# Performance work log

Measured on AMD Instinct MI355X. Metric: run time of the kernel, lower is better.

## Reference

```python
import jax, jax.numpy as jnp
import numpy as np

N_QUBITS = 8


def _rot_mats(p):
    # p: (n, 3) -> per-qubit 2x2 unitary RX(p2) @ RZ(p1) @ RY(p0), shape (n, 2, 2)
    a, b, c = 0.5 * p[:, 0], 0.5 * p[:, 1], 0.5 * p[:, 2]
    zc = jnp.zeros_like(a).astype(jnp.complex64)
    ca, sa = jnp.cos(a), jnp.sin(a)
    ry = jnp.stack([jnp.stack([ca, -sa], -1), jnp.stack([sa, ca], -1)], -2).astype(jnp.complex64)
    eb = jnp.exp(-1j * b)
    rz = jnp.stack([jnp.stack([eb, zc], -1), jnp.stack([zc, jnp.conj(eb)], -1)], -2)
    cc = jnp.cos(c).astype(jnp.complex64)
    sc = -1j * jnp.sin(c)
    rx = jnp.stack([jnp.stack([cc, sc], -1), jnp.stack([sc, cc], -1)], -2)
    return rx @ rz @ ry


def _qgate(x, params):
    # Batched statevector simulation of the PennyLane circuit.
    # x: (B, n) RX-encoding angles; params: (depth, n, 3). Wire 0 = most-significant bit.
    B, n = x.shape
    half = 0.5 * x
    # RX(x)|0> per qubit = [cos(x/2), -i sin(x/2)]
    amps = jnp.stack([jnp.cos(half).astype(jnp.complex64), (-1j) * jnp.sin(half)], axis=-1)  # (B,n,2)
    state = amps[:, 0]  # (B, 2)
    for q in range(1, n):
        state = (state[:, :, None] * amps[:, q][:, None, :]).reshape(B, -1)
    for d in range(params.shape[0]):
        U = _rot_mats(params[d])  # (n, 2, 2)
        for w in range(n):
            s = state.reshape(B, 2 ** w, 2, -1)
            s = jnp.einsum('ab,xlbr->xlar', U[w], s)
            state = s.reshape(B, -1)
        for c in range(n - 1):  # CNOT chain (c controls c+1)
            s = state.reshape(B, 2 ** c, 2, 2, -1)
            s = jnp.stack([s[:, :, 0], s[:, :, 1, ::-1]], axis=2)
            state = s.reshape(B, -1)
    probs = state.real ** 2 + state.imag ** 2  # (B, 2**n)
    k = np.arange(2 ** n)
    signs = (1.0 - 2.0 * (((k[None, :] >> (n - 1 - np.arange(n)[:, None])) & 1))).astype(np.float32)
    return probs @ jnp.asarray(signs).T  # (B, n) Pauli-Z expvals


def _apply_gate_list(x, params_list):
    # params_list: (n_gates, depth, n, 3); gates applied sequentially
    for g in range(params_list.shape[0]):
        x = _qgate(x, params_list[g])
    return x


def setup_inputs() -> dict:
    key = jax.random.key(0)
    ks = jax.random.split(key, 10)
    T, B, D, H, P, NQ, DP = 32, 64, 512, 512, 64, N_QUBITS, 2
    inputs = jax.random.normal(ks[0], (T, B, D), jnp.float32)
    W_proj = jax.random.normal(ks[1], (P, D + H), jnp.float32) / jnp.sqrt(jnp.float32(D + H))
    b_proj = jax.random.normal(ks[2], (P,), jnp.float32) * 0.01
    W_toq = jax.random.normal(ks[3], (NQ, P), jnp.float32) / jnp.sqrt(jnp.float32(P))
    W_q2h = jax.random.normal(ks[4], (H, NQ), jnp.float32) / jnp.sqrt(jnp.float32(NQ))
    f_params = jax.random.normal(ks[5], (DP, DP, NQ, 3), jnp.float32)
    i_params = jax.random.normal(ks[6], (DP, DP, NQ, 3), jnp.float32)
    g_params = jax.random.normal(ks[7], (DP, DP, NQ, 3), jnp.float32)
    o_params = jax.random.normal(ks[8], (DP, DP, NQ, 3), jnp.float32)
    return dict(inputs=inputs, W_proj=W_proj, b_proj=b_proj, W_toq=W_toq, W_q2h=W_q2h,
                f_params=f_params, i_params=i_params, g_params=g_params, o_params=o_params)


def reference(inputs, W_proj, b_proj, W_toq, W_q2h, f_params, i_params, g_params, o_params):
    B = inputs.shape[1]
    H = W_q2h.shape[0]

    def step(carry, x):
        hx, cx = carry
        combined = jnp.concatenate([x, hx], axis=1)          # (B, D+H)
        proj = combined @ W_proj.T + b_proj                   # (B, P)
        qin = proj @ W_toq.T                                  # (B, NQ)
        f = jax.nn.sigmoid(_apply_gate_list(qin, f_params) @ W_q2h.T)
        i = jax.nn.sigmoid(_apply_gate_list(qin, i_params) @ W_q2h.T)
        g = jnp.tanh(_apply_gate_list(qin, g_params) @ W_q2h.T)
        o = jax.nn.sigmoid(_apply_gate_list(qin, o_params) @ W_q2h.T)
        cx2 = f * cx + i * g
        hx2 = o * jnp.tanh(cx2)
        return (hx2, cx2), hx2

    init = (jnp.zeros((B, H), inputs.dtype), jnp.zeros((B, H), inputs.dtype))
    (hx, cx), stacked = jax.lax.scan(step, init, inputs)
    return stacked, hx, cx
```

## Files before the change

kernel.cpp:

```cpp
#include <hip/hip_runtime.h>
#include <math.h>

#define T_STEPS 32
#define BATCH 64

#define WS_WXQ 0
#define WS_WHQ 4096
#define WS_BQ  8192
#define WS_U   8208
#define WS_XQ  9232
#define WS_AB  25616

typedef float v2f __attribute__((ext_vector_type(2)));
typedef unsigned int u32x2 __attribute__((ext_vector_type(2)));
typedef __fp16 half4v __attribute__((ext_vector_type(4)));
typedef float f32x4 __attribute__((ext_vector_type(4)));

struct c32 { float x, y; };
__device__ __forceinline__ c32 cmul(c32 a, c32 b){ return {a.x*b.x - a.y*b.y, a.x*b.y + a.y*b.x}; }
__device__ __forceinline__ c32 cadd(c32 a, c32 b){ return {a.x+b.x, a.y+b.y}; }

__device__ __forceinline__ v2f mkv(float x, float y){ v2f r; r.x = x; r.y = y; return r; }
__device__ __forceinline__ v2f cmulv(v2f a, v2f b){
    return mkv(a.x, a.x) * b + mkv(-a.y, a.y) * mkv(b.y, b.x);
}
__device__ __forceinline__ float fast_sigmoid(float x){ return 1.f/(1.f + __expf(-x)); }
__device__ __forceinline__ float fast_tanh(float x){ float e = __expf(2.f*x); return 1.f - 2.f/(e+1.f); }

template<int C> __device__ __forceinline__ float dppf(float v){
    return __int_as_float(__builtin_amdgcn_mov_dpp(__float_as_int(v), C, 0xF, 0xF, true));
}
__device__ __forceinline__ float swap16(float v, int lane){
#if __has_builtin(__builtin_amdgcn_permlane16_swap)
    u32x2 r = __builtin_amdgcn_permlane16_swap(__float_as_uint(v), __float_as_uint(v), false, false);
    return __uint_as_float((lane & 16) ? r.x : r.y);
#else
    return __shfl_xor(v, 16);
#endif
}
__device__ __forceinline__ float swap32(float v, int lane){
#if __has_builtin(__builtin_amdgcn_permlane32_swap)
    u32x2 r = __builtin_amdgcn_permlane32_swap(__float_as_uint(v), __float_as_uint(v), false, false);
    return __uint_as_float((lane & 32) ? r.x : r.y);
#else
    return __shfl_xor(v, 32);
#endif
}
template<int LM> __device__ __forceinline__ float lanexor(float v, int lane){
    if constexpr (LM == 1)       return dppf<0xB1>(v);
    else if constexpr (LM == 2)  return dppf<0x4E>(v);
    else if constexpr (LM == 4)  return dppf<0x1B>(dppf<0x141>(v));
    else if constexpr (LM == 8)  return dppf<0x128>(v);
    else if constexpr (LM == 16) return swap16(v, lane);
    else                         return swap32(v, lane);
}
__device__ __forceinline__ float rdl(float v, int l){
    return __int_as_float(__builtin_amdgcn_readlane(__float_as_int(v), l));
}
__device__ __forceinline__ void fsincos(float rev, float* s, float* c){
#if __has_builtin(__builtin_amdgcn_sinf) && __has_builtin(__builtin_amdgcn_cosf)
    *s = __builtin_amdgcn_sinf(rev);
    *c = __builtin_amdgcn_cosf(rev);
#else
    __sincosf(rev * 6.2831853071795864f, s, c);
#endif
}

__device__ __forceinline__ void rot_u(const float* p3, float* dst){
    float a = 0.5f * p3[0], b = 0.5f * p3[1], c = 0.5f * p3[2];
    float ca = cosf(a), sa = sinf(a);
    float cb = cosf(b), sb = sinf(b);
    float cc = cosf(c), sc = sinf(c);
    c32 eb  = {cb, -sb};
    c32 ebc = {cb,  sb};
    c32 scx = {0.f, -sc};
    c32 m00 = { eb.x * ca,  eb.y * ca};
    c32 m01 = {-eb.x * sa, -eb.y * sa};
    c32 m10 = { ebc.x * sa, ebc.y * sa};
    c32 m11 = { ebc.x * ca, ebc.y * ca};
    c32 U00 = cadd(c32{cc * m00.x, cc * m00.y}, cmul(scx, m10));
    c32 U01 = cadd(c32{cc * m01.x, cc * m01.y}, cmul(scx, m11));
    c32 U10 = cadd(cmul(scx, m00), c32{cc * m10.x, cc * m10.y});
    c32 U11 = cadd(cmul(scx, m01), c32{cc * m11.x, cc * m11.y});
    dst[0] = U00.x; dst[1] = U00.y; dst[2] = U01.x; dst[3] = U01.y;
    dst[4] = U10.x; dst[5] = U10.y; dst[6] = U11.x; dst[7] = U11.y;
}

__global__ void precompute_kernel(const float* __restrict__ W_proj,
                                  const float* __restrict__ b_proj,
                                  const float* __restrict__ W_toq,
                                  const float* __restrict__ fP, const float* __restrict__ iP,
                                  const float* __restrict__ gP, const float* __restrict__ oP,
                                  float* __restrict__ ws)
{
    int tid = threadIdx.x;
    int blk = blockIdx.x;
    if (blk < 32) {
        int idx = blk * 256 + tid;
        int q = idx >> 10, dd = idx & 1023;
        float acc = 0.f;
        for (int p = 0; p < 64; ++p) acc += W_toq[q * 64 + p] * W_proj[p * 1024 + dd];
        if (dd < 512) ws[WS_WXQ + q * 512 + dd] = acc;
        else          ws[WS_WHQ + q * 512 + (dd - 512)] = acc;
        if (idx < 8) {
            float a2 = 0.f;
            for (int p = 0; p < 64; ++p) a2 += W_toq[idx * 64 + p] * b_proj[p];
            ws[WS_BQ + idx] = a2;
        }
    } else if (blk == 32) {
        if (tid < 128) {
            int gt = tid >> 5, rest = tid & 31;
            const float* P = (gt == 0) ? fP : (gt == 1) ? iP : (gt == 2) ? gP : oP;
            int g = (rest >> 4) & 1, d = (rest >> 3) & 1, w = rest & 7;
            rot_u(P + (((g * 2 + d) * 8 + w) * 3), ws + WS_U + tid * 8);
        }
    } else {
        __shared__ float sW[8][8];
        int combo = blk - 33;
        int gt = combo >> 1, gl = combo & 1;
        if (tid < 8) {
            const float* P = (gt == 0) ? fP : (gt == 1) ? iP : (gt == 2) ? gP : oP;
            rot_u(P + (((gl * 2 + 1) * 8 + tid) * 3), &sW[tid][0]);
        }
        __syncthreads();
        int rp = tid >> 4, rr = tid & 15;
        c32 pa = {1.f, 0.f};
        #pragma unroll
        for (int w = 0; w < 4; ++w) {
            int i = (rp >> (3 - w)) & 1, j = (rr >> (3 - w)) & 1;
            c32 e = {sW[w][(i * 2 + j) * 2], sW[w][(i * 2 + j) * 2 + 1]};
            pa = cmul(pa, e);
        }
        ws[WS_AB + combo * 1024 + tid * 2]     = pa.x;
        ws[WS_AB + combo * 1024 + tid * 2 + 1] = pa.y;
        c32 pb = {1.f, 0.f};
        #pragma unroll
        for (int w = 4; w < 8; ++w) {
            int i = (rp >> (7 - w)) & 1, j = (rr >> (7 - w)) & 1;
            c32 e = {sW[w][(i * 2 + j) * 2], sW[w][(i * 2 + j) * 2 + 1]};
            pb = cmul(pb, e);
        }
        ws[WS_AB + combo * 1024 + 512 + tid * 2]     = pb.x;
        ws[WS_AB + combo * 1024 + 512 + tid * 2 + 1] = pb.y;
    }
}

__global__ void xq_kernel(const float* __restrict__ inputs, float* __restrict__ ws)
{
    __shared__ float xs[512];
    int row = blockIdx.x;
    int tid = threadIdx.x;
    xs[tid]       = inputs[row * 512 + tid];
    xs[tid + 256] = inputs[row * 512 + 256 + tid];
    __syncthreads();
    int g = tid >> 5, j = tid & 31;
    const float* w = ws + WS_WXQ + g * 512;
    float acc = 0.f;
    #pragma unroll 4
    for (int i = 0; i < 16; ++i) acc += xs[j + 32 * i] * w[j + 32 * i];
    acc += __shfl_xor(acc, 1);  acc += __shfl_xor(acc, 2);
    acc += __shfl_xor(acc, 4);  acc += __shfl_xor(acc, 8);
    acc += __shfl_xor(acc, 16);
    if (j == 0) ws[WS_XQ + row * 8 + g] = acc + ws[WS_BQ + g];
}

__global__ __launch_bounds__(256, 1)
void recurrence_kernel(const float* __restrict__ W_q2h,
                       const float* __restrict__ ws,
                       float* __restrict__ out)
{
    __shared__ __align__(16) float sU[1024];
    __shared__ __align__(16) float sXq[T_STEPS * 8];
    __shared__ __align__(16) float sexpW[4][8];
    __shared__ __align__(16) float qpartW[4][8];
    __shared__ __align__(16) float sH[T_STEPS * 512];

    int tid = threadIdx.x;
    int b   = blockIdx.x;
    int wv  = tid >> 6;
    int lane = tid & 63;
    int l = lane;

    for (int i = tid; i < 1024; i += 256) sU[i] = ws[WS_U + i];
    sXq[tid] = ws[WS_XQ + ((tid >> 3) * 64 + b) * 8 + (tid & 7)];
    if (tid < 32) ((float*)qpartW)[tid] = 0.f;

    v2f wha2[4], whb2[4];
    #pragma unroll
    for (int j = 0; j < 4; ++j) {
        wha2[j] = mkv(ws[WS_WHQ + (2*j) * 512 + tid],       ws[WS_WHQ + (2*j+1) * 512 + tid]);
        whb2[j] = mkv(ws[WS_WHQ + (2*j) * 512 + tid + 256], ws[WS_WHQ + (2*j+1) * 512 + tid + 256]);
    }
    v2f w2hp[8];
    {
        float4 a0 = *(const float4*)&W_q2h[tid * 8];
        float4 a1 = *(const float4*)&W_q2h[tid * 8 + 4];
        float4 b0 = *(const float4*)&W_q2h[(tid + 256) * 8];
        float4 b1 = *(const float4*)&W_q2h[(tid + 256) * 8 + 4];
        w2hp[0] = mkv(a0.x, b0.x); w2hp[1] = mkv(a0.y, b0.y);
        w2hp[2] = mkv(a0.z, b0.z); w2hp[3] = mkv(a0.w, b0.w);
        w2hp[4] = mkv(a1.x, b1.x); w2hp[5] = mkv(a1.y, b1.y);
        w2hp[6] = mkv(a1.z, b1.z); w2hp[7] = mkv(a1.w, b1.w);
    }

    half4v ArT[2], AiT[2], nAiT[2], Brf[2], Bif[2], nBif[2];
    {
        int q4 = lane >> 4, n = lane & 15;
        #pragma unroll
        for (int gl = 0; gl < 2; ++gl) {
            const float* Ab = ws + WS_AB + (wv * 2 + gl) * 1024;
            const float* Bb = Ab + 512;
            #pragma unroll
            for (int j = 0; j < 4; ++j) {
                int k = 4 * q4 + j;
                float ar = Ab[(n * 16 + k) * 2], ai = Ab[(n * 16 + k) * 2 + 1];
                float br = Bb[(n * 16 + k) * 2], bi = Bb[(n * 16 + k) * 2 + 1];
                ArT[gl][j]  = (__fp16)ar;  AiT[gl][j] = (__fp16)ai;  nAiT[gl][j] = (__fp16)(-ai);
                Brf[gl][j]  = (__fp16)br;  Bif[gl][j] = (__fp16)bi;  nBif[gl][j] = (__fp16)(-bi);
            }
        }
    }

    __syncthreads();

    v2f sA0[2], sB0[2], sA1[2], sB1[2], sA5[2], sB5[2], sA6[2], sB6[2], sA7[2], sB7[2];
    v2f A2a[2], B2a[2], A2b[2], B2b[2];
    v2f A3a[2], B3a[2], A3b[2], B3b[2];
    v2f A4a[2], B4a[2], A4b[2], B4b[2];
    {
        int s0 = (l >> 5) & 1;
        int s1 = ((l >> 5) ^ (l >> 4)) & 1;
        int s5 = ((l >> 3) ^ (l >> 2)) & 1;
        int s6 = ((l >> 2) ^ (l >> 1)) & 1;
        int s7 = ((l >> 1) ^ l) & 1;
        int L4 = (l >> 4) & 1;
        int L3 = (l >> 3) & 1;
        #pragma unroll
        for (int gl = 0; gl < 2; ++gl) {
            const float* d0 = sU + (wv * 32 + gl * 16) * 8;
            auto colA = [&](int q, int c){ const float* m = d0 + q * 8 + c * 4; return mkv(m[0], m[1]); };
            auto colB = [&](int q, int c){ const float* m = d0 + q * 8 + c * 4; return mkv(m[3 - c * 4 + c * 4 + 3 - 3 + 3], 0.f); };
            #define CA(q,c) mkv(d0[(q)*8 + (c)*4 + 0], d0[(q)*8 + (c)*4 + 1])
            #define CB(q,c) mkv(d0[(q)*8 + (c)*4 + 3], -d0[(q)*8 + (c)*4 + 2])
            sA0[gl] = s0 ? CA(0,1) : CA(0,0);  sB0[gl] = s0 ? CB(0,1) : CB(0,0);
            sA1[gl] = s1 ? CA(1,1) : CA(1,0);  sB1[gl] = s1 ? CB(1,1) : CB(1,0);
            sA5[gl] = s5 ? CA(5,1) : CA(5,0);  sB5[gl] = s5 ? CB(5,1) : CB(5,0);
            sA6[gl] = s6 ? CA(6,1) : CA(6,0);  sB6[gl] = s6 ? CB(6,1) : CB(6,0);
            sA7[gl] = s7 ? CA(7,1) : CA(7,0);  sB7[gl] = s7 ? CB(7,1) : CB(7,0);
            A2a[gl] = L4 ? CA(2,1) : CA(2,0);  B2a[gl] = L4 ? CB(2,1) : CB(2,0);
            A2b[gl] = L4 ? CA(2,0) : CA(2,1);  B2b[gl] = L4 ? CB(2,0) : CB(2,1);
            A3a[gl] = CA(3,0);                 B3a[gl] = CB(3,0);
            A3b[gl] = CA(3,1);                 B3b[gl] = CB(3,1);
            A4a[gl] = L3 ? CA(4,1) : CA(4,0);  B4a[gl] = L3 ? CB(4,1) : CB(4,0);
            A4b[gl] = L3 ? CA(4,0) : CA(4,1);  B4b[gl] = L3 ? CB(4,0) : CB(4,1);
            #undef CA
            #undef CB
            (void)colA; (void)colB;
        }
    }
    float sg[6];
    #pragma unroll
    for (int st = 0; st < 6; ++st) sg[st] = ((l >> st) & 1) ? -1.f : 1.f;

    const float REVC = 0.07957747154594767f;
    const f32x4 zacc = {0.f, 0.f, 0.f, 0.f};
    float c0 = 0.f, c1 = 0.f, h0 = 0.f, h1 = 0.f;

    for (int t = 0; t < T_STEPS; ++t) {
        float ang[8];
        {
            const v2f* qw = (const v2f*)qpartW;
            const v2f* xq2 = (const v2f*)&sXq[t * 8];
            #pragma unroll
            for (int j = 0; j < 4; ++j) {
                v2f s_ = ((qw[j] + qw[4 + j]) + (qw[8 + j] + qw[12 + j]) + xq2[j]) * REVC;
                ang[2 * j] = s_.x; ang[2 * j + 1] = s_.y;
            }
        }

        float e[8];
        #pragma unroll
        for (int gl = 0; gl < 2; ++gl) {
            float sh[8], ch[8];
            #pragma unroll
            for (int q = 0; q < 8; ++q) fsincos(ang[q], &sh[q], &ch[q]);

            v2f u0 = ch[0] * sA0[gl] + sh[0] * sB0[gl];
            v2f u1 = ch[1] * sA1[gl] + sh[1] * sB1[gl];
            v2f u5 = ch[5] * sA5[gl] + sh[5] * sB5[gl];
            v2f u6 = ch[6] * sA6[gl] + sh[6] * sB6[gl];
            v2f u7 = ch[7] * sA7[gl] + sh[7] * sB7[gl];
            v2f u2a = ch[2] * A2a[gl] + sh[2] * B2a[gl];
            v2f u2b = ch[2] * A2b[gl] + sh[2] * B2b[gl];
            v2f u3a = ch[3] * A3a[gl] + sh[3] * B3a[gl];
            v2f u3b = ch[3] * A3b[gl] + sh[3] * B3b[gl];
            v2f u4a = ch[4] * A4a[gl] + sh[4] * B4a[gl];
            v2f u4b = ch[4] * A4b[gl] + sh[4] * B4b[gl];

            v2f hi = cmulv(u0, u1);
            v2f lo = cmulv(cmulv(u5, u6), u7);
            v2f hilo = cmulv(hi, lo);
            v2f u23_0 = cmulv(u2a, u3a);
            v2f u23_1 = cmulv(u2a, u3b);
            v2f u23_2 = cmulv(u2b, u3b);
            v2f u23_3 = cmulv(u2b, u3a);
            v2f mid0 = cmulv(u23_0, u4a);
            v2f mid1 = cmulv(u23_1, u4b);
            v2f mid2 = cmulv(u23_2, u4a);
            v2f mid3 = cmulv(u23_3, u4b);
            v2f a0 = cmulv(hilo, mid0);
            v2f a1 = cmulv(hilo, mid1);
            v2f a2 = cmulv(hilo, mid2);
            v2f a3 = cmulv(hilo, mid3);

            half4v Sr, Si;
            Sr[0] = (__fp16)a0.x; Sr[1] = (__fp16)a1.x; Sr[2] = (__fp16)a2.x; Sr[3] = (__fp16)a3.x;
            Si[0] = (__fp16)a0.y; Si[1] = (__fp16)a1.y; Si[2] = (__fp16)a2.y; Si[3] = (__fp16)a3.y;

            f32x4 TrT = __builtin_amdgcn_mfma_f32_16x16x16f16(Sr, ArT[gl], zacc, 0, 0, 0);
            TrT = __builtin_amdgcn_mfma_f32_16x16x16f16(Si, nAiT[gl], TrT, 0, 0, 0);
            f32x4 TiT = __builtin_amdgcn_mfma_f32_16x16x16f16(Sr, AiT[gl], zacc, 0, 0, 0);
            TiT = __builtin_amdgcn_mfma_f32_16x16x16f16(Si, ArT[gl], TiT, 0, 0, 0);
            half4v TrH, TiH;
            #pragma unroll
            for (int j = 0; j < 4; ++j) { TrH[j] = (__fp16)TrT[j]; TiH[j] = (__fp16)TiT[j]; }
            f32x4 Xr = __builtin_amdgcn_mfma_f32_16x16x16f16(Brf[gl], TrH, zacc, 0, 0, 0);
            Xr = __builtin_amdgcn_mfma_f32_16x16x16f16(nBif[gl], TiH, Xr, 0, 0, 0);
            f32x4 Xi = __builtin_amdgcn_mfma_f32_16x16x16f16(Brf[gl], TiH, zacc, 0, 0, 0);
            Xi = __builtin_amdgcn_mfma_f32_16x16x16f16(Bif[gl], TrH, Xi, 0, 0, 0);

            float p0 = Xr[0]*Xr[0] + Xi[0]*Xi[0];
            float p1 = Xr[1]*Xr[1] + Xi[1]*Xi[1];
            float p2 = Xr[2]*Xr[2] + Xi[2]*Xi[2];
            float p3 = Xr[3]*Xr[3] + Xi[3]*Xi[3];
            float w0v = (p0 + p1) + (p2 + p3);
            float w6v = (p0 + p1) - (p2 + p3);
            float w7v = (p0 - p1) - (p2 - p3);
            #define WHT_STAGE(LM, ST) { float v_; \
                v_ = lanexor<LM>(w0v, lane); w0v = __builtin_fmaf(sg[ST], w0v, v_); \
                v_ = lanexor<LM>(w6v, lane); w6v = __builtin_fmaf(sg[ST], w6v, v_); \
                v_ = lanexor<LM>(w7v, lane); w7v = __builtin_fmaf(sg[ST], w7v, v_); }
            WHT_STAGE(1, 0) WHT_STAGE(2, 1) WHT_STAGE(4, 2)
            WHT_STAGE(8, 3) WHT_STAGE(16, 4) WHT_STAGE(32, 5)
            #undef WHT_STAGE
            e[0] = rdl(w0v, 8);  e[1] = rdl(w0v, 12); e[2] = rdl(w0v, 14);
            e[3] = rdl(w0v, 15); e[4] = rdl(w0v, 47); e[5] = rdl(w0v, 63);
            e[6] = rdl(w6v, 63); e[7] = rdl(w7v, 63);
            if (gl == 0) {
                #pragma unroll
                for (int q = 0; q < 8; ++q) ang[q] = e[q] * REVC;
            }
        }
        if (lane == 0) {
            float4 e0v; e0v.x = e[0]; e0v.y = e[1]; e0v.z = e[2]; e0v.w = e[3];
            float4 e1v; e1v.x = e[4]; e1v.y = e[5]; e1v.z = e[6]; e1v.w = e[7];
            *(float4*)&sexpW[wv][0] = e0v;
            *(float4*)&sexpW[wv][4] = e1v;
        }
        __syncthreads();

        {
            v2f pre[4];
            #pragma unroll
            for (int g = 0; g < 4; ++g) {
                float4 ea = *(const float4*)&sexpW[g][0];
                float4 eb2 = *(const float4*)&sexpW[g][4];
                v2f acc = ea.x * w2hp[0] + ea.y * w2hp[1] + ea.z * w2hp[2] + ea.w * w2hp[3]
                        + eb2.x * w2hp[4] + eb2.y * w2hp[5] + eb2.z * w2hp[6] + eb2.w * w2hp[7];
                pre[g] = acc;
            }
            float f0 = fast_sigmoid(pre[0].x), i0 = fast_sigmoid(pre[1].x);
            float g0 = fast_tanh(pre[2].x),    o0 = fast_sigmoid(pre[3].x);
            c0 = f0 * c0 + i0 * g0;  h0 = o0 * fast_tanh(c0);
            float f1 = fast_sigmoid(pre[0].y), i1 = fast_sigmoid(pre[1].y);
            float g1 = fast_tanh(pre[2].y),    o1 = fast_sigmoid(pre[3].y);
            c1 = f1 * c1 + i1 * g1;  h1 = o1 * fast_tanh(c1);
            sH[t * 512 + tid]       = h0;
            sH[t * 512 + tid + 256] = h1;
        }

        {
            v2f pp[4];
            #pragma unroll
            for (int j = 0; j < 4; ++j) pp[j] = wha2[j] * h0 + whb2[j] * h1;
            #pragma unroll
            for (int j = 0; j < 4; ++j) {
                pp[j] += mkv(lanexor<1>(pp[j].x, lane), lanexor<1>(pp[j].y, lane));
                pp[j] += mkv(lanexor<2>(pp[j].x, lane), lanexor<2>(pp[j].y, lane));
                pp[j] += mkv(lanexor<4>(pp[j].x, lane), lanexor<4>(pp[j].y, lane));
            }
            int sel = lane & 7;
            float y = (sel == 0) ? pp[0].x : (sel == 1) ? pp[0].y
                    : (sel == 2) ? pp[1].x : (sel == 3) ? pp[1].y
                    : (sel == 4) ? pp[2].x : (sel == 5) ? pp[2].y
                    : (sel == 6) ? pp[3].x : pp[3].y;
            y += lanexor<8>(y, lane);
            y += swap16(y, lane);
            y += swap32(y, lane);
            if (lane < 8) qpartW[wv][lane] = y;
        }
        __syncthreads();
    }

    {
        const float4* src = (const float4*)sH;
        float4* dst = (float4*)out;
        #pragma unroll
        for (int k = 0; k < 16; ++k) {
            int i = k * 256 + tid;
            int t = i >> 7, h4 = i & 127;
            dst[(t * 64 + b) * 128 + h4] = src[i];
        }
    }
    float* hx_out = out + (size_t)T_STEPS * 64 * 512;
    float* cx_out = hx_out + 64 * 512;
    hx_out[b * 512 + tid]       = h0;
    hx_out[b * 512 + tid + 256] = h1;
    cx_out[b * 512 + tid]       = c0;
    cx_out[b * 512 + tid + 256] = c1;
}

extern "C" void kernel_launch(void* const* d_in, const int* in_sizes, int n_in,
                              void* d_out, int out_size, void* d_ws, size_t ws_size,
                              hipStream_t stream)
{
    const float* inputs = (const float*)d_in[0];
    const float* W_proj = (const float*)d_in[1];
    const float* b_proj = (const float*)d_in[2];
    const float* W_toq  = (const float*)d_in[3];
    const float* W_q2h  = (const float*)d_in[4];
    const float* fP     = (const float*)d_in[5];
    const float* iP     = (const float*)d_in[6];
    const float* gP     = (const float*)d_in[7];
    const float* oP     = (const float*)d_in[8];
    float* ws  = (float*)d_ws;
    float* out = (float*)d_out;

    precompute_kernel<<<41, 256, 0, stream>>>(W_proj, b_proj, W_toq, fP, iP, gP, oP, ws);
    xq_kernel<<<T_STEPS * BATCH, 256, 0, stream>>>(inputs, ws);
    recurrence_kernel<<<BATCH, 256, 0, stream>>>(W_q2h, ws, out);
}
```

Baseline: 150.2 us.

## Fuse precompute, input projection and recurrence into a single kernel

Replaces the three launches (weight precompute, per-row input projection, recurrence) with one kernel in which every batch block redundantly computes the folded W_toq·W_proj weights, the rotation matrices and the Kronecker A/B factors into registers and shared memory. It then stages its own inputs in shared memory and computes the per-step qubit angles locally. This removes two kernel launches and the workspace round-trips, at the cost of redundant per-block setup work (a 64-deep loop over W_proj reads). The MFMA chains are also split into independent products that are summed afterwards, to shorten dependency latency.

```diff
diff --git a/kernel.cpp b/kernel.cpp
--- a/kernel.cpp
+++ b/kernel.cpp
@@ -3,13 +3,6 @@
 
 #define T_STEPS 32
 #define BATCH 64
-
-#define WS_WXQ 0
-#define WS_WHQ 4096
-#define WS_BQ  8192
-#define WS_U   8208
-#define WS_XQ  9232
-#define WS_AB  25616
 
 typedef float v2f __attribute__((ext_vector_type(2)));
 typedef unsigned int u32x2 __attribute__((ext_vector_type(2)));
@@ -86,88 +79,15 @@
     dst[4] = U10.x; dst[5] = U10.y; dst[6] = U11.x; dst[7] = U11.y;
 }
 
-__global__ void precompute_kernel(const float* __restrict__ W_proj,
-                                  const float* __restrict__ b_proj,
-                                  const float* __restrict__ W_toq,
-                                  const float* __restrict__ fP, const float* __restrict__ iP,
-                                  const float* __restrict__ gP, const float* __restrict__ oP,
-                                  float* __restrict__ ws)
-{
-    int tid = threadIdx.x;
-    int blk = blockIdx.x;
-    if (blk < 32) {
-        int idx = blk * 256 + tid;
-        int q = idx >> 10, dd = idx & 1023;
-        float acc = 0.f;
-        for (int p = 0; p < 64; ++p) acc += W_toq[q * 64 + p] * W_proj[p * 1024 + dd];
-        if (dd < 512) ws[WS_WXQ + q * 512 + dd] = acc;
-        else          ws[WS_WHQ + q * 512 + (dd - 512)] = acc;
-        if (idx < 8) {
-            float a2 = 0.f;
-            for (int p = 0; p < 64; ++p) a2 += W_toq[idx * 64 + p] * b_proj[p];
-            ws[WS_BQ + idx] = a2;
-        }
-    } else if (blk == 32) {
-        if (tid < 128) {
-            int gt = tid >> 5, rest = tid & 31;
-            const float* P = (gt == 0) ? fP : (gt == 1) ? iP : (gt == 2) ? gP : oP;
-            int g = (rest >> 4) & 1, d = (rest >> 3) & 1, w = rest & 7;
-            rot_u(P + (((g * 2 + d) * 8 + w) * 3), ws + WS_U + tid * 8);
-        }
-    } else {
-        __shared__ float sW[8][8];
-        int combo = blk - 33;
-        int gt = combo >> 1, gl = combo & 1;
-        if (tid < 8) {
-            const float* P = (gt == 0) ? fP : (gt == 1) ? iP : (gt == 2) ? gP : oP;
-            rot_u(P + (((gl * 2 + 1) * 8 + tid) * 3), &sW[tid][0]);
-        }
-        __syncthreads();
-        int rp = tid >> 4, rr = tid & 15;
-        c32 pa = {1.f, 0.f};
-        #pragma unroll
-        for (int w = 0; w < 4; ++w) {
-            int i = (rp >> (3 - w)) & 1, j = (rr >> (3 - w)) & 1;
-            c32 e = {sW[w][(i * 2 + j) * 2], sW[w][(i * 2 + j) * 2 + 1]};
-            pa = cmul(pa, e);
-        }
-        ws[WS_AB + combo * 1024 + tid * 2]     = pa.x;
-        ws[WS_AB + combo * 1024 + tid * 2 + 1] = pa.y;
-        c32 pb = {1.f, 0.f};
-        #pragma unroll
-        for (int w = 4; w < 8; ++w) {
-            int i = (rp >> (7 - w)) & 1, j = (rr >> (7 - w)) & 1;
-            c32 e = {sW[w][(i * 2 + j) * 2], sW[w][(i * 2 + j) * 2 + 1]};
-            pb = cmul(pb, e);
-        }
-        ws[WS_AB + combo * 1024 + 512 + tid * 2]     = pb.x;
-        ws[WS_AB + combo * 1024 + 512 + tid * 2 + 1] = pb.y;
-    }
-}
-
-__global__ void xq_kernel(const float* __restrict__ inputs, float* __restrict__ ws)
-{
-    __shared__ float xs[512];
-    int row = blockIdx.x;
-    int tid = threadIdx.x;
-    xs[tid]       = inputs[row * 512 + tid];
-    xs[tid + 256] = inputs[row * 512 + 256 + tid];
-    __syncthreads();
-    int g = tid >> 5, j = tid & 31;
-    const float* w = ws + WS_WXQ + g * 512;
-    float acc = 0.f;
-    #pragma unroll 4
-    for (int i = 0; i < 16; ++i) acc += xs[j + 32 * i] * w[j + 32 * i];
-    acc += __shfl_xor(acc, 1);  acc += __shfl_xor(acc, 2);
-    acc += __shfl_xor(acc, 4);  acc += __shfl_xor(acc, 8);
-    acc += __shfl_xor(acc, 16);
-    if (j == 0) ws[WS_XQ + row * 8 + g] = acc + ws[WS_BQ + g];
-}
-
 __global__ __launch_bounds__(256, 1)
-void recurrence_kernel(const float* __restrict__ W_q2h,
-                       const float* __restrict__ ws,
-                       float* __restrict__ out)
+void fused_kernel(const float* __restrict__ inputs,
+                  const float* __restrict__ W_proj,
+                  const float* __restrict__ b_proj,
+                  const float* __restrict__ W_toq,
+                  const float* __restrict__ W_q2h,
+                  const float* __restrict__ fP, const float* __restrict__ iP,
+                  const float* __restrict__ gP, const float* __restrict__ oP,
+                  float* __restrict__ out)
 {
     __shared__ __align__(16) float sU[1024];
     __shared__ __align__(16) float sXq[T_STEPS * 8];
@@ -175,21 +95,56 @@
     __shared__ __align__(16) float qpartW[4][8];
     __shared__ __align__(16) float sH[T_STEPS * 512];
 
+    float* sAB = sH;
+
     int tid = threadIdx.x;
     int b   = blockIdx.x;
     int wv  = tid >> 6;
     int lane = tid & 63;
     int l = lane;
 
-    for (int i = tid; i < 1024; i += 256) sU[i] = ws[WS_U + i];
-    sXq[tid] = ws[WS_XQ + ((tid >> 3) * 64 + b) * 8 + (tid & 7)];
+    if (tid < 128) {
+        int gt = tid >> 5, rest = tid & 31;
+        const float* P = (gt == 0) ? fP : (gt == 1) ? iP : (gt == 2) ? gP : oP;
+        int g = (rest >> 4) & 1, d = (rest >> 3) & 1, w = rest & 7;
+        rot_u(P + (((g * 2 + d) * 8 + w) * 3), sU + tid * 8);
+    }
     if (tid < 32) ((float*)qpartW)[tid] = 0.f;
 
+    float wha[8], whb[8]; float4 wxq4[4]; float bq = 0.f;
+    #pragma unroll
+    for (int q = 0; q < 8; ++q) { wha[q] = 0.f; whb[q] = 0.f; }
+    #pragma unroll
+    for (int k = 0; k < 4; ++k) { wxq4[k].x = 0.f; wxq4[k].y = 0.f; wxq4[k].z = 0.f; wxq4[k].w = 0.f; }
+    {
+        int jj = tid & 31, gq = tid >> 5;
+        for (int p = 0; p < 64; ++p) {
+            float av = W_proj[p * 1024 + 512 + tid];
+            float bv = W_proj[p * 1024 + 768 + tid];
+            #pragma unroll
+            for (int q = 0; q < 8; ++q) {
+                float wt = W_toq[q * 64 + p];
+                wha[q] = fmaf(wt, av, wha[q]);
+                whb[q] = fmaf(wt, bv, whb[q]);
+            }
+            float wtg = W_toq[gq * 64 + p];
+            const float4* wrow = (const float4*)&W_proj[p * 1024 + jj * 16];
+            #pragma unroll
+            for (int k = 0; k < 4; ++k) {
+                float4 wv4 = wrow[k];
+                wxq4[k].x = fmaf(wtg, wv4.x, wxq4[k].x);
+                wxq4[k].y = fmaf(wtg, wv4.y, wxq4[k].y);
+                wxq4[k].z = fmaf(wtg, wv4.z, wxq4[k].z);
+                wxq4[k].w = fmaf(wtg, wv4.w, wxq4[k].w);
+            }
+            bq = fmaf(wtg, b_proj[p], bq);
+        }
+    }
     v2f wha2[4], whb2[4];
     #pragma unroll
     for (int j = 0; j < 4; ++j) {
-        wha2[j] = mkv(ws[WS_WHQ + (2*j) * 512 + tid],       ws[WS_WHQ + (2*j+1) * 512 + tid]);
-        whb2[j] = mkv(ws[WS_WHQ + (2*j) * 512 + tid + 256], ws[WS_WHQ + (2*j+1) * 512 + tid + 256]);
+        wha2[j] = mkv(wha[2 * j], wha[2 * j + 1]);
+        whb2[j] = mkv(whb[2 * j], whb[2 * j + 1]);
     }
     v2f w2hp[8];
     {
@@ -203,12 +158,45 @@
         w2hp[6] = mkv(a1.z, b1.z); w2hp[7] = mkv(a1.w, b1.w);
     }
 
+    __syncthreads();
+
+    {
+        int combo = tid >> 5;
+        int gt = combo >> 1, gl2 = combo & 1;
+        const float* d1 = sU + (gt * 32 + gl2 * 16 + 8) * 8;
+        int jj = tid & 31;
+        #pragma unroll
+        for (int it = 0; it < 8; ++it) {
+            int idx = jj + 32 * it;
+            int rp = idx >> 4, rr = idx & 15;
+            c32 pa = {1.f, 0.f};
+            #pragma unroll
+            for (int w = 0; w < 4; ++w) {
+                int i2 = (rp >> (3 - w)) & 1, j2 = (rr >> (3 - w)) & 1;
+                c32 e2 = { d1[w * 8 + (i2 * 2 + j2) * 2], d1[w * 8 + (i2 * 2 + j2) * 2 + 1] };
+                pa = cmul(pa, e2);
+            }
+            sAB[combo * 1024 + idx * 2]     = pa.x;
+            sAB[combo * 1024 + idx * 2 + 1] = pa.y;
+            c32 pb = {1.f, 0.f};
+            #pragma unroll
+            for (int w = 4; w < 8; ++w) {
+                int i2 = (rp >> (7 - w)) & 1, j2 = (rr >> (7 - w)) & 1;
+                c32 e2 = { d1[w * 8 + (i2 * 2 + j2) * 2], d1[w * 8 + (i2 * 2 + j2) * 2 + 1] };
+                pb = cmul(pb, e2);
+            }
+            sAB[combo * 1024 + 512 + idx * 2]     = pb.x;
+            sAB[combo * 1024 + 512 + idx * 2 + 1] = pb.y;
+        }
+    }
+    __syncthreads();
+
     half4v ArT[2], AiT[2], nAiT[2], Brf[2], Bif[2], nBif[2];
     {
         int q4 = lane >> 4, n = lane & 15;
         #pragma unroll
         for (int gl = 0; gl < 2; ++gl) {
-            const float* Ab = ws + WS_AB + (wv * 2 + gl) * 1024;
+            const float* Ab = sAB + (wv * 2 + gl) * 1024;
             const float* Bb = Ab + 512;
             #pragma unroll
             for (int j = 0; j < 4; ++j) {
@@ -220,8 +208,6 @@
             }
         }
     }
-
-    __syncthreads();
 
     v2f sA0[2], sB0[2], sA1[2], sB1[2], sA5[2], sB5[2], sA6[2], sB6[2], sA7[2], sB7[2];
     v2f A2a[2], B2a[2], A2b[2], B2b[2];
@@ -238,8 +224,6 @@
         #pragma unroll
         for (int gl = 0; gl < 2; ++gl) {
             const float* d0 = sU + (wv * 32 + gl * 16) * 8;
-            auto colA = [&](int q, int c){ const float* m = d0 + q * 8 + c * 4; return mkv(m[0], m[1]); };
-            auto colB = [&](int q, int c){ const float* m = d0 + q * 8 + c * 4; return mkv(m[3 - c * 4 + c * 4 + 3 - 3 + 3], 0.f); };
             #define CA(q,c) mkv(d0[(q)*8 + (c)*4 + 0], d0[(q)*8 + (c)*4 + 1])
             #define CB(q,c) mkv(d0[(q)*8 + (c)*4 + 3], -d0[(q)*8 + (c)*4 + 2])
             sA0[gl] = s0 ? CA(0,1) : CA(0,0);  sB0[gl] = s0 ? CB(0,1) : CB(0,0);
@@ -255,12 +239,44 @@
             A4b[gl] = L3 ? CA(4,0) : CA(4,1);  B4b[gl] = L3 ? CB(4,0) : CB(4,1);
             #undef CA
             #undef CB
-            (void)colA; (void)colB;
         }
     }
     float sg[6];
     #pragma unroll
     for (int st = 0; st < 6; ++st) sg[st] = ((l >> st) & 1) ? -1.f : 1.f;
+
+    __syncthreads();
+
+    {
+        const float4* inp4 = (const float4*)inputs;
+        float4* sh4 = (float4*)sH;
+        #pragma unroll
+        for (int k = 0; k < 16; ++k) {
+            int i = k * 256 + tid;
+            int t = i >> 7, c4 = i & 127;
+            sh4[i] = inp4[(t * 64 + b) * 128 + c4];
+        }
+    }
+    __syncthreads();
+
+    {
+        int gq = tid >> 5, jj = tid & 31;
+        for (int t2 = 0; t2 < T_STEPS; ++t2) {
+            const float4* row = (const float4*)&sH[t2 * 512 + jj * 16];
+            float acc = 0.f;
+            #pragma unroll
+            for (int k = 0; k < 4; ++k) {
+                float4 xv = row[k];
+                float4 wv4 = wxq4[k];
+                acc += xv.x * wv4.x + xv.y * wv4.y + xv.z * wv4.z + xv.w * wv4.w;
+            }
+            acc += __shfl_xor(acc, 1);  acc += __shfl_xor(acc, 2);
+            acc += __shfl_xor(acc, 4);  acc += __shfl_xor(acc, 8);
+            acc += __shfl_xor(acc, 16);
+            if (jj == 0) sXq[t2 * 8 + gq] = acc + bq;
+        }
+    }
+    __syncthreads();
 
     const float REVC = 0.07957747154594767f;
     const f32x4 zacc = {0.f, 0.f, 0.f, 0.f};
@@ -317,17 +333,21 @@
             Sr[0] = (__fp16)a0.x; Sr[1] = (__fp16)a1.x; Sr[2] = (__fp16)a2.x; Sr[3] = (__fp16)a3.x;
             Si[0] = (__fp16)a0.y; Si[1] = (__fp16)a1.y; Si[2] = (__fp16)a2.y; Si[3] = (__fp16)a3.y;
 
-            f32x4 TrT = __builtin_amdgcn_mfma_f32_16x16x16f16(Sr, ArT[gl], zacc, 0, 0, 0);
-            TrT = __builtin_amdgcn_mfma_f32_16x16x16f16(Si, nAiT[gl], TrT, 0, 0, 0);
-            f32x4 TiT = __builtin_amdgcn_mfma_f32_16x16x16f16(Sr, AiT[gl], zacc, 0, 0, 0);
-            TiT = __builtin_amdgcn_mfma_f32_16x16x16f16(Si, ArT[gl], TiT, 0, 0, 0);
+            f32x4 Tr0 = __builtin_amdgcn_mfma_f32_16x16x16f16(Sr, ArT[gl], zacc, 0, 0, 0);
+            f32x4 Tr1 = __builtin_amdgcn_mfma_f32_16x16x16f16(Si, nAiT[gl], zacc, 0, 0, 0);
+            f32x4 Ti0 = __builtin_amdgcn_mfma_f32_16x16x16f16(Sr, AiT[gl], zacc, 0, 0, 0);
+            f32x4 Ti1 = __builtin_amdgcn_mfma_f32_16x16x16f16(Si, ArT[gl], zacc, 0, 0, 0);
+            f32x4 TrT = Tr0 + Tr1;
+            f32x4 TiT = Ti0 + Ti1;
             half4v TrH, TiH;
             #pragma unroll
             for (int j = 0; j < 4; ++j) { TrH[j] = (__fp16)TrT[j]; TiH[j] = (__fp16)TiT[j]; }
-            f32x4 Xr = __builtin_amdgcn_mfma_f32_16x16x16f16(Brf[gl], TrH, zacc, 0, 0, 0);
-            Xr = __builtin_amdgcn_mfma_f32_16x16x16f16(nBif[gl], TiH, Xr, 0, 0, 0);
-            f32x4 Xi = __builtin_amdgcn_mfma_f32_16x16x16f16(Brf[gl], TiH, zacc, 0, 0, 0);
-            Xi = __builtin_amdgcn_mfma_f32_16x16x16f16(Bif[gl], TrH, Xi, 0, 0, 0);
+            f32x4 Xr0 = __builtin_amdgcn_mfma_f32_16x16x16f16(Brf[gl], TrH, zacc, 0, 0, 0);
+            f32x4 Xr1 = __builtin_amdgcn_mfma_f32_16x16x16f16(nBif[gl], TiH, zacc, 0, 0, 0);
+            f32x4 Xi0 = __builtin_amdgcn_mfma_f32_16x16x16f16(Brf[gl], TiH, zacc, 0, 0, 0);
+            f32x4 Xi1 = __builtin_amdgcn_mfma_f32_16x16x16f16(Bif[gl], TrH, zacc, 0, 0, 0);
+            f32x4 Xr = Xr0 + Xr1;
+            f32x4 Xi = Xi0 + Xi1;
 
             float p0 = Xr[0]*Xr[0] + Xi[0]*Xi[0];
             float p1 = Xr[1]*Xr[1] + Xi[1]*Xi[1];
@@ -433,10 +453,9 @@
     const float* iP     = (const float*)d_in[6];
     const float* gP     = (const float*)d_in[7];
     const float* oP     = (const float*)d_in[8];
-    float* ws  = (float*)d_ws;
     float* out = (float*)d_out;
-
-    precompute_kernel<<<41, 256, 0, stream>>>(W_proj, b_proj, W_toq, fP, iP, gP, oP, ws);
-    xq_kernel<<<T_STEPS * BATCH, 256, 0, stream>>>(inputs, ws);
-    recurrence_kernel<<<BATCH, 256, 0, stream>>>(W_q2h, ws, out);
-}
+    (void)d_ws; (void)ws_size; (void)in_sizes; (void)n_in; (void)out_size;
+
+    fused_kernel<<<BATCH, 256, 0, stream>>>(inputs, W_proj, b_proj, W_toq, W_q2h,
+                                            fP, iP, gP, oP, out);
+}
```

Result: slower. 169.0 us (+12.5%).

## Replace shuffle Walsh-Hadamard reduction with MFMA sign matmul and stream outputs directly

Applied to the files above, without the earlier changes.

The per-step Pauli-Z expectation reduction, previously a six-stage lane-xor Walsh-Hadamard butterfly, becomes one f16 MFMA against a precomputed sign matrix plus sign scaling and two permlane swaps. Complex products are reassociated to share hilo*u4 terms. f32-to-f16 packing uses cvt_pkrtz. The REVC scale is folded into the precomputed xq and qpart values. The hidden-state history now goes straight to global memory each step instead of through a 64KB LDS buffer and a final copy. The goal is a shorter serial per-step critical path. The cost is extra fp16 rounding of probabilities and round-toward-zero conversions.

```diff
diff --git a/kernel.cpp b/kernel.cpp
--- a/kernel.cpp
+++ b/kernel.cpp
@@ -13,6 +13,7 @@
 
 typedef float v2f __attribute__((ext_vector_type(2)));
 typedef unsigned int u32x2 __attribute__((ext_vector_type(2)));
+typedef __fp16 half2v __attribute__((ext_vector_type(2)));
 typedef __fp16 half4v __attribute__((ext_vector_type(4)));
 typedef float f32x4 __attribute__((ext_vector_type(4)));
 
@@ -26,6 +27,17 @@
 }
 __device__ __forceinline__ float fast_sigmoid(float x){ return 1.f/(1.f + __expf(-x)); }
 __device__ __forceinline__ float fast_tanh(float x){ float e = __expf(2.f*x); return 1.f - 2.f/(e+1.f); }
+
+__device__ __forceinline__ half4v pk4(float a, float b, float c, float d){
+#if __has_builtin(__builtin_amdgcn_cvt_pkrtz)
+    half2v lo = __builtin_amdgcn_cvt_pkrtz(a, b);
+    half2v hi = __builtin_amdgcn_cvt_pkrtz(c, d);
+    return __builtin_shufflevector(lo, hi, 0, 1, 2, 3);
+#else
+    half4v r; r[0] = (__fp16)a; r[1] = (__fp16)b; r[2] = (__fp16)c; r[3] = (__fp16)d;
+    return r;
+#endif
+}
 
 template<int C> __device__ __forceinline__ float dppf(float v){
     return __int_as_float(__builtin_amdgcn_mov_dpp(__float_as_int(v), C, 0xF, 0xF, true));
@@ -161,7 +173,7 @@
     acc += __shfl_xor(acc, 1);  acc += __shfl_xor(acc, 2);
     acc += __shfl_xor(acc, 4);  acc += __shfl_xor(acc, 8);
     acc += __shfl_xor(acc, 16);
-    if (j == 0) ws[WS_XQ + row * 8 + g] = acc + ws[WS_BQ + g];
+    if (j == 0) ws[WS_XQ + row * 8 + g] = (acc + ws[WS_BQ + g]) * 0.07957747154594767f;
 }
 
 __global__ __launch_bounds__(256, 1)
@@ -173,7 +185,6 @@
     __shared__ __align__(16) float sXq[T_STEPS * 8];
     __shared__ __align__(16) float sexpW[4][8];
     __shared__ __align__(16) float qpartW[4][8];
-    __shared__ __align__(16) float sH[T_STEPS * 512];
 
     int tid = threadIdx.x;
     int b   = blockIdx.x;
@@ -238,8 +249,6 @@
         #pragma unroll
         for (int gl = 0; gl < 2; ++gl) {
             const float* d0 = sU + (wv * 32 + gl * 16) * 8;
-            auto colA = [&](int q, int c){ const float* m = d0 + q * 8 + c * 4; return mkv(m[0], m[1]); };
-            auto colB = [&](int q, int c){ const float* m = d0 + q * 8 + c * 4; return mkv(m[3 - c * 4 + c * 4 + 3 - 3 + 3], 0.f); };
             #define CA(q,c) mkv(d0[(q)*8 + (c)*4 + 0], d0[(q)*8 + (c)*4 + 1])
             #define CB(q,c) mkv(d0[(q)*8 + (c)*4 + 3], -d0[(q)*8 + (c)*4 + 2])
             sA0[gl] = s0 ? CA(0,1) : CA(0,0);  sB0[gl] = s0 ? CB(0,1) : CB(0,0);
@@ -255,14 +264,27 @@
             A4b[gl] = L3 ? CA(4,0) : CA(4,1);  B4b[gl] = L3 ? CB(4,0) : CB(4,1);
             #undef CA
             #undef CB
-            (void)colA; (void)colB;
-        }
-    }
-    float sg[6];
-    #pragma unroll
-    for (int st = 0; st < 6; ++st) sg[st] = ((l >> st) & 1) ? -1.f : 1.f;
+        }
+    }
 
     const float REVC = 0.07957747154594767f;
+
+    half4v Bsgn; f32x4 SHsgn, SHsgnR;
+    {
+        int q = lane & 15;
+        int g4 = lane >> 4;
+        int mlo = (q < 4) ? 0 : (q == 4) ? 8 : (q == 5) ? 12 : (q == 6) ? 14 : (q == 7) ? 15 : 0;
+        int mhi = (q == 0) ? 8 : (q == 1) ? 12 : (q == 2) ? 14 : 15;
+        #pragma unroll
+        for (int j = 0; j < 4; ++j) {
+            int k = 4 * g4 + j;
+            float bs = (q < 8) ? ((__builtin_popcount(k & mlo) & 1) ? -1.f : 1.f) : 0.f;
+            Bsgn[j] = (__fp16)bs;
+            SHsgn[j]  = (__builtin_popcount(k & mhi) & 1) ? -1.f : 1.f;
+            SHsgnR[j] = SHsgn[j] * REVC;
+        }
+    }
+
     const f32x4 zacc = {0.f, 0.f, 0.f, 0.f};
     float c0 = 0.f, c1 = 0.f, h0 = 0.f, h1 = 0.f;
 
@@ -273,7 +295,7 @@
             const v2f* xq2 = (const v2f*)&sXq[t * 8];
             #pragma unroll
             for (int j = 0; j < 4; ++j) {
-                v2f s_ = ((qw[j] + qw[4 + j]) + (qw[8 + j] + qw[12 + j]) + xq2[j]) * REVC;
+                v2f s_ = (qw[j] + qw[4 + j]) + (qw[8 + j] + qw[12 + j]) + xq2[j];
                 ang[2 * j] = s_.x; ang[2 * j + 1] = s_.y;
             }
         }
@@ -300,55 +322,43 @@
             v2f hi = cmulv(u0, u1);
             v2f lo = cmulv(cmulv(u5, u6), u7);
             v2f hilo = cmulv(hi, lo);
+            v2f hl_a = cmulv(hilo, u4a);
+            v2f hl_b = cmulv(hilo, u4b);
             v2f u23_0 = cmulv(u2a, u3a);
             v2f u23_1 = cmulv(u2a, u3b);
             v2f u23_2 = cmulv(u2b, u3b);
             v2f u23_3 = cmulv(u2b, u3a);
-            v2f mid0 = cmulv(u23_0, u4a);
-            v2f mid1 = cmulv(u23_1, u4b);
-            v2f mid2 = cmulv(u23_2, u4a);
-            v2f mid3 = cmulv(u23_3, u4b);
-            v2f a0 = cmulv(hilo, mid0);
-            v2f a1 = cmulv(hilo, mid1);
-            v2f a2 = cmulv(hilo, mid2);
-            v2f a3 = cmulv(hilo, mid3);
-
-            half4v Sr, Si;
-            Sr[0] = (__fp16)a0.x; Sr[1] = (__fp16)a1.x; Sr[2] = (__fp16)a2.x; Sr[3] = (__fp16)a3.x;
-            Si[0] = (__fp16)a0.y; Si[1] = (__fp16)a1.y; Si[2] = (__fp16)a2.y; Si[3] = (__fp16)a3.y;
+            v2f a0 = cmulv(u23_0, hl_a);
+            v2f a1 = cmulv(u23_1, hl_b);
+            v2f a2 = cmulv(u23_2, hl_a);
+            v2f a3 = cmulv(u23_3, hl_b);
+
+            half4v Sr = pk4(a0.x, a1.x, a2.x, a3.x);
+            half4v Si = pk4(a0.y, a1.y, a2.y, a3.y);
 
             f32x4 TrT = __builtin_amdgcn_mfma_f32_16x16x16f16(Sr, ArT[gl], zacc, 0, 0, 0);
             TrT = __builtin_amdgcn_mfma_f32_16x16x16f16(Si, nAiT[gl], TrT, 0, 0, 0);
             f32x4 TiT = __builtin_amdgcn_mfma_f32_16x16x16f16(Sr, AiT[gl], zacc, 0, 0, 0);
             TiT = __builtin_amdgcn_mfma_f32_16x16x16f16(Si, ArT[gl], TiT, 0, 0, 0);
-            half4v TrH, TiH;
-            #pragma unroll
-            for (int j = 0; j < 4; ++j) { TrH[j] = (__fp16)TrT[j]; TiH[j] = (__fp16)TiT[j]; }
+            half4v TrH = pk4(TrT[0], TrT[1], TrT[2], TrT[3]);
+            half4v TiH = pk4(TiT[0], TiT[1], TiT[2], TiT[3]);
             f32x4 Xr = __builtin_amdgcn_mfma_f32_16x16x16f16(Brf[gl], TrH, zacc, 0, 0, 0);
             Xr = __builtin_amdgcn_mfma_f32_16x16x16f16(nBif[gl], TiH, Xr, 0, 0, 0);
             f32x4 Xi = __builtin_amdgcn_mfma_f32_16x16x16f16(Brf[gl], TiH, zacc, 0, 0, 0);
             Xi = __builtin_amdgcn_mfma_f32_16x16x16f16(Bif[gl], TrH, Xi, 0, 0, 0);
 
-            float p0 = Xr[0]*Xr[0] + Xi[0]*Xi[0];
-            float p1 = Xr[1]*Xr[1] + Xi[1]*Xi[1];
-            float p2 = Xr[2]*Xr[2] + Xi[2]*Xi[2];
-            float p3 = Xr[3]*Xr[3] + Xi[3]*Xi[3];
-            float w0v = (p0 + p1) + (p2 + p3);
-            float w6v = (p0 + p1) - (p2 + p3);
-            float w7v = (p0 - p1) - (p2 - p3);
-            #define WHT_STAGE(LM, ST) { float v_; \
-                v_ = lanexor<LM>(w0v, lane); w0v = __builtin_fmaf(sg[ST], w0v, v_); \
-                v_ = lanexor<LM>(w6v, lane); w6v = __builtin_fmaf(sg[ST], w6v, v_); \
-                v_ = lanexor<LM>(w7v, lane); w7v = __builtin_fmaf(sg[ST], w7v, v_); }
-            WHT_STAGE(1, 0) WHT_STAGE(2, 1) WHT_STAGE(4, 2)
-            WHT_STAGE(8, 3) WHT_STAGE(16, 4) WHT_STAGE(32, 5)
-            #undef WHT_STAGE
-            e[0] = rdl(w0v, 8);  e[1] = rdl(w0v, 12); e[2] = rdl(w0v, 14);
-            e[3] = rdl(w0v, 15); e[4] = rdl(w0v, 47); e[5] = rdl(w0v, 63);
-            e[6] = rdl(w6v, 63); e[7] = rdl(w7v, 63);
+            f32x4 P = Xr * Xr + Xi * Xi;
+            half4v Pf = pk4(P[0], P[1], P[2], P[3]);
+            f32x4 Cm = __builtin_amdgcn_mfma_f32_16x16x16f16(Pf, Bsgn, zacc, 0, 0, 0);
+            f32x4 Mm = Cm * ((gl == 0) ? SHsgnR : SHsgn);
+            float v = (Mm[0] + Mm[1]) + (Mm[2] + Mm[3]);
+            v += swap16(v, lane);
+            v += swap32(v, lane);
+            e[0] = rdl(v, 0); e[1] = rdl(v, 1); e[2] = rdl(v, 2); e[3] = rdl(v, 3);
+            e[4] = rdl(v, 4); e[5] = rdl(v, 5); e[6] = rdl(v, 6); e[7] = rdl(v, 7);
             if (gl == 0) {
                 #pragma unroll
-                for (int q = 0; q < 8; ++q) ang[q] = e[q] * REVC;
+                for (int q = 0; q < 8; ++q) ang[q] = e[q];
             }
         }
         if (lane == 0) {
@@ -375,8 +385,8 @@
             float f1 = fast_sigmoid(pre[0].y), i1 = fast_sigmoid(pre[1].y);
             float g1 = fast_tanh(pre[2].y),    o1 = fast_sigmoid(pre[3].y);
             c1 = f1 * c1 + i1 * g1;  h1 = o1 * fast_tanh(c1);
-            sH[t * 512 + tid]       = h0;
-            sH[t * 512 + tid + 256] = h1;
+            out[(t * 64 + b) * 512 + tid]       = h0;
+            out[(t * 64 + b) * 512 + tid + 256] = h1;
         }
 
         {
@@ -397,21 +407,11 @@
             y += lanexor<8>(y, lane);
             y += swap16(y, lane);
             y += swap32(y, lane);
-            if (lane < 8) qpartW[wv][lane] = y;
+            if (lane < 8) qpartW[wv][lane] = y * REVC;
         }
         __syncthreads();
     }
 
-    {
-        const float4* src = (const float4*)sH;
-        float4* dst = (float4*)out;
-        #pragma unroll
-        for (int k = 0; k < 16; ++k) {
-            int i = k * 256 + tid;
-            int t = i >> 7, h4 = i & 127;
-            dst[(t * 64 + b) * 128 + h4] = src[i];
-        }
-    }
     float* hx_out = out + (size_t)T_STEPS * 64 * 512;
     float* cx_out = hx_out + 64 * 512;
     hx_out[b * 512 + tid]       = h0;
```

New measurement: 141.5 us. 5.8% less time.
